# Kernel tuning notes

Measured on AMD Instinct MI355X. Metric: run time of the kernel, lower is better.

The kernel has to match this reference:

```python
import jax, jax.numpy as jnp
import numpy as np
import math

T = 2048; HID = 2048; H = 16; KV = 8; G = H // KV; D = 128
GH = 128; BS = 64; NB = T // BS
EPS = 1e-6; RATIO = 0.2; SCALE = 1.0 / math.sqrt(D)


def _rope_tables(length, dim, theta=1000000.0):
    inv = 1.0 / (theta ** (np.arange(0, dim, 2, dtype=np.float32) / dim))
    f = np.outer(np.arange(length, dtype=np.float32), inv)
    emb = np.concatenate([f, f], axis=-1)
    return jnp.asarray(np.cos(emb)), jnp.asarray(np.sin(emb))


def _rot_half(x):
    d = x.shape[-1] // 2
    return jnp.concatenate([-x[..., d:], x[..., :d]], axis=-1)


def _apply_rope(x, cos, sin):
    # x: [T, nH, D], cos/sin: [T, D] broadcast over head dim
    return x * cos[:, None, :] + _rot_half(x) * sin[:, None, :]


def _rmsnorm(x, w, eps=EPS):
    xf = x.astype(jnp.float32)
    v = jnp.mean(xf * xf, axis=-1, keepdims=True)
    return (w * (xf * jax.lax.rsqrt(v + eps))).astype(x.dtype)


def setup_inputs() -> dict:
    key = jax.random.key(0)
    ks = jax.random.split(key, 8)
    s = 0.02
    hidden_states = jax.random.normal(ks[0], (T, HID), jnp.float32)
    Wq = jax.random.normal(ks[1], (HID, H * D), jnp.float32) * s
    Wk = jax.random.normal(ks[2], (HID, KV * D), jnp.float32) * s
    Wv = jax.random.normal(ks[3], (HID, KV * D), jnp.float32) * s
    Wo = jax.random.normal(ks[4], (H * D, HID), jnp.float32) * s
    q_norm_w = jnp.ones((D,), jnp.float32)
    k_norm_w = jnp.ones((D,), jnp.float32)
    gate_wq = jax.random.normal(ks[5], (D, GH), jnp.float32) * s
    gate_wk = jax.random.normal(ks[6], (D, GH), jnp.float32) * s
    cos, sin = _rope_tables(T, D)
    cos_gq, sin_gq = _rope_tables(T, GH)
    cos_blk, sin_blk = _rope_tables(NB, GH)
    # causal block mask: query t may attend to key block j iff j <= t // BS
    block_attention_mask = (jnp.arange(T)[:, None] // BS) >= jnp.arange(NB)[None, :]
    return dict(hidden_states=hidden_states, Wq=Wq, Wk=Wk, Wv=Wv, Wo=Wo,
                q_norm_w=q_norm_w, k_norm_w=k_norm_w, gate_wq=gate_wq, gate_wk=gate_wk,
                cos=cos, sin=sin, cos_gq=cos_gq, sin_gq=sin_gq,
                cos_blk=cos_blk, sin_blk=sin_blk,
                block_attention_mask=block_attention_mask)


def reference(hidden_states, Wq, Wk, Wv, Wo, q_norm_w, k_norm_w, gate_wq, gate_wk,
              cos, sin, cos_gq, sin_gq, cos_blk, sin_blk, block_attention_mask):
    q = (hidden_states @ Wq).reshape(T, H, D)
    k = (hidden_states @ Wk).reshape(T, KV, D)
    v = (hidden_states @ Wv).reshape(T, KV, D)
    q = _rmsnorm(q, q_norm_w)
    k = _rmsnorm(k, k_norm_w)

    # ---- gate network on un-roped q/k: q-head avg-pool to KV heads, k avg-pool per block ----
    q_pool = q.reshape(T, KV, G, D).mean(axis=2)            # [T, KV, D]
    gq = _apply_rope(q_pool @ gate_wq, cos_gq, sin_gq)      # [T, KV, GH]
    k_blk = k.reshape(NB, BS, KV, D).mean(axis=1)           # [NB, KV, D]
    gk = _apply_rope(k_blk @ gate_wk, cos_blk, sin_blk)     # [NB, KV, GH]
    gate_scores = jnp.einsum('tkg,nkg->ktn', gq, gk) / math.sqrt(GH)  # [KV, T, NB]
    predict_mask = jnp.where(block_attention_mask[None], gate_scores, -1e9)

    # ---- main attention (RoPE + GQA causal softmax attention) ----
    qr = _apply_rope(q, cos, sin)
    kr = _apply_rope(k, cos, sin)
    kr_rep = jnp.repeat(kr, G, axis=1)                      # [T, H, D]
    v_rep = jnp.repeat(v, G, axis=1)
    logits = jnp.einsum('thd,shd->hts', qr, kr_rep) * SCALE  # [H, T, T]
    causal = jnp.tril(jnp.ones((T, T), bool))
    logits = jnp.where(causal[None], logits, -jnp.inf)
    probs = jax.nn.softmax(logits, axis=-1)
    attn_output = jnp.einsum('hts,shd->thd', probs, v_rep).reshape(T, H * D) @ Wo

    # ---- pooled ground-truth block mask: attention mass per key block ----
    pooled = probs.reshape(H, T, NB, BS).sum(axis=-1)        # [H, T, NB]
    gt = pooled.reshape(KV, G, T, NB).max(axis=1)            # max_pool3d over head groups -> [KV,T,NB]
    gt = jnp.where(block_attention_mask[None], gt, 0.0)
    gt = gt / (gt.sum(axis=-1, keepdims=True) + 1e-9)

    # ---- KLDiv gate loss on the tail slice (bsz = 1) ----
    start = int(T * RATIO)
    tgt = gt[:, start:, :]                                   # [KV, L, NB]
    logp = jax.nn.log_softmax(predict_mask[:, start:, :], axis=-1)
    safe_t = jnp.where(tgt > 0, tgt, 1.0)
    kl = jnp.where(tgt > 0, tgt * (jnp.log(safe_t) - logp), 0.0)
    gate_loss = kl.reshape(KV, -1).mean(axis=-1).sum()       # KLDivLoss(reduction='mean') per kv head, summed, /bsz(=1)
    return attn_output, gate_loss
```

## Files before the change

### kernel.cpp

```cpp
#include <hip/hip_runtime.h>

#define T_ 2048
#define HID_ 2048
#define H_ 16
#define KV_ 8
#define G_ 2
#define D_ 128
#define GH_ 128
#define BS_ 64
#define NB_ 32
#define START_ 409
#define TG0_ 384
#define SCALE_ 0.08838834764831845f
#define MFIX_ 8.0f

typedef __attribute__((ext_vector_type(8))) short short8_t;
typedef __attribute__((ext_vector_type(4))) float float4_t;
typedef __attribute__((ext_vector_type(8))) unsigned short ushort8_t;
typedef __attribute__((ext_vector_type(4))) unsigned short ushort4_t;

__device__ __forceinline__ float wave_sum(float v) {
#pragma unroll
  for (int o = 32; o > 0; o >>= 1) v += __shfl_xor(v, o, 64);
  return v;
}
__device__ __forceinline__ unsigned short f2bf(float x) {
  unsigned int u = __float_as_uint(x);
  unsigned int r = (u + 0x7fffu + ((u >> 16) & 1u)) >> 16;
  return (unsigned short)r;
}

__device__ __forceinline__ void gload16(const void* g, void* l) {
  __builtin_amdgcn_global_load_lds((const __attribute__((address_space(1))) unsigned int*)g,
                                   (__attribute__((address_space(3))) unsigned int*)l, 16, 0, 0);
}

__device__ __forceinline__ void castT_dev(const float* __restrict__ in,
                                          unsigned short* __restrict__ out, int K, int N,
                                          int ldin, int bx, int by,
                                          unsigned short (*tile)[72], int tid) {
  int k0 = by * 64, n0 = bx * 64;
  int tx = tid & 63, ty4 = tid >> 6;
#pragma unroll
  for (int i = 0; i < 16; ++i) {
    int ky = ty4 * 16 + i;
    tile[tx][ky] = f2bf(in[(size_t)(k0 + ky) * ldin + n0 + tx]);
  }
  __syncthreads();
#pragma unroll
  for (int i = 0; i < 16; ++i) {
    int ny = ty4 * 16 + i;
    out[(size_t)(n0 + ny) * K + k0 + tx] = tile[ny][tx];
  }
}

__global__ __launch_bounds__(256) void castT(const float* __restrict__ in,
                                             unsigned short* __restrict__ out,
                                             int K, int N, int ldin) {
  __shared__ unsigned short tile[64][72];
  castT_dev(in, out, K, N, ldin, blockIdx.x, blockIdx.y, tile, threadIdx.x);
}

__global__ __launch_bounds__(256) void prep_cast(const float* __restrict__ hs,
                                                 const float* __restrict__ Wq,
                                                 const float* __restrict__ Wk,
                                                 const float* __restrict__ Wv,
                                                 const float* __restrict__ Wo,
                                                 const float* __restrict__ gwq,
                                                 const float* __restrict__ gwk,
                                                 unsigned short* __restrict__ hsb,
                                                 unsigned short* __restrict__ WqkvT,
                                                 unsigned short* __restrict__ WoT,
                                                 unsigned short* __restrict__ gwqT,
                                                 unsigned short* __restrict__ gwkT) {
  __shared__ unsigned short tile[64][72];
  int id = blockIdx.x, tid = threadIdx.x;
  if (id < 4096) {
    int i = id * 256 + tid;
    float4 v = ((const float4*)hs)[i];
    ushort4_t o = {f2bf(v.x), f2bf(v.y), f2bf(v.z), f2bf(v.w)};
    *(ushort4_t*)(hsb + (size_t)i * 4) = o;
  } else if (id < 5120) {
    int t = id - 4096;
    castT_dev(Wq, WqkvT, 2048, 2048, 2048, t & 31, t >> 5, tile, tid);
  } else if (id < 5632) {
    int t = id - 5120;
    castT_dev(Wk, WqkvT + (size_t)2048 * 2048, 2048, 1024, 1024, t & 15, t >> 4, tile, tid);
  } else if (id < 6144) {
    int t = id - 5632;
    castT_dev(Wv, WqkvT + (size_t)3072 * 2048, 2048, 1024, 1024, t & 15, t >> 4, tile, tid);
  } else if (id < 7168) {
    int t = id - 6144;
    castT_dev(Wo, WoT, 2048, 2048, 2048, t & 31, t >> 5, tile, tid);
  } else if (id < 7172) {
    int t = id - 7168;
    castT_dev(gwq, gwqT, 128, 128, 128, t & 1, t >> 1, tile, tid);
  } else {
    int t = id - 7172;
    castT_dev(gwk, gwkT, 128, 128, 128, t & 1, t >> 1, tile, tid);
  }
}

__device__ __forceinline__ void gemm_body(const unsigned short* __restrict__ A,
                                          const unsigned short* __restrict__ Bt,
                                          float* __restrict__ C,
                                          int M, int N, int K, int ldc, int bx, int by,
                                          unsigned short* As, unsigned short* Bs) {
  int tid = threadIdx.x;
  int wid = tid >> 6, lane = tid & 63;
  int quad = lane >> 4, l16 = lane & 15;
  int wm = wid & 1, wn = wid >> 1;
  int m0 = by * 128, n0 = bx * 128;
  const unsigned short* gA[4];
  const unsigned short* gB[4];
#pragma unroll
  for (int it = 0; it < 4; ++it) {
    int line = wid * 32 + it * 8 + (lane >> 3);
    int chunk = (lane & 7) ^ (line & 7);
    gA[it] = A + (size_t)(m0 + line) * K + chunk * 8;
    gB[it] = Bt + (size_t)(n0 + line) * K + chunk * 8;
  }
  float4_t acc[4][4];
#pragma unroll
  for (int i = 0; i < 4; ++i)
#pragma unroll
    for (int j = 0; j < 4; ++j) acc[i][j] = (float4_t){0.f, 0.f, 0.f, 0.f};
  int nk = K >> 6;
#pragma unroll
  for (int it = 0; it < 4; ++it) {
    gload16(gA[it], As + (wid * 32 + it * 8) * 64);
    gload16(gB[it], Bs + (wid * 32 + it * 8) * 64);
  }
  for (int t = 0; t < nk; ++t) {
    __syncthreads();
    if (t + 1 < nk) {
      int bo = ((t + 1) & 1) * 8192;
#pragma unroll
      for (int it = 0; it < 4; ++it) {
        gload16(gA[it] + (t + 1) * 64, As + bo + (wid * 32 + it * 8) * 64);
        gload16(gB[it] + (t + 1) * 64, Bs + bo + (wid * 32 + it * 8) * 64);
      }
    }
    const unsigned short* Asc = As + (t & 1) * 8192;
    const unsigned short* Bsc = Bs + (t & 1) * 8192;
    short8_t a[2][4], b[2][4];
#pragma unroll
    for (int ks = 0; ks < 2; ++ks) {
      int sw = ((ks * 4 + quad) ^ (l16 & 7)) * 8;
#pragma unroll
      for (int i = 0; i < 4; ++i) {
        a[ks][i] = *(const short8_t*)&Asc[(wm * 64 + i * 16 + l16) * 64 + sw];
        b[ks][i] = *(const short8_t*)&Bsc[(wn * 64 + i * 16 + l16) * 64 + sw];
      }
    }
#pragma unroll
    for (int ks = 0; ks < 2; ++ks)
#pragma unroll
      for (int i = 0; i < 4; ++i)
#pragma unroll
        for (int j = 0; j < 4; ++j)
          acc[i][j] = __builtin_amdgcn_mfma_f32_16x16x32_bf16(a[ks][i], b[ks][j], acc[i][j], 0, 0, 0);
  }
#pragma unroll
  for (int i = 0; i < 4; ++i)
#pragma unroll
    for (int j = 0; j < 4; ++j)
#pragma unroll
      for (int reg = 0; reg < 4; ++reg)
        C[(size_t)(m0 + wm * 64 + i * 16 + quad * 4 + reg) * ldc + n0 + wn * 64 + j * 16 + l16] =
            acc[i][j][reg];
}

__global__ __launch_bounds__(256) void gemm_bf16_v3(const unsigned short* __restrict__ A,
                                                    const unsigned short* __restrict__ Bt,
                                                    float* __restrict__ C,
                                                    int M, int N, int K, int ldc) {
  __shared__ unsigned short As[2 * 128 * 64];
  __shared__ unsigned short Bs[2 * 128 * 64];
  gemm_body(A, Bt, C, M, N, K, ldc, blockIdx.x, blockIdx.y, As, Bs);
}

__global__ __launch_bounds__(256) void gemm_gates(const unsigned short* __restrict__ Aq,
                                                  const unsigned short* __restrict__ Bq,
                                                  float* __restrict__ Cq,
                                                  const unsigned short* __restrict__ Ak,
                                                  const unsigned short* __restrict__ Bk,
                                                  float* __restrict__ Ck) {
  __shared__ unsigned short As[2 * 128 * 64];
  __shared__ unsigned short Bs[2 * 128 * 64];
  int y = blockIdx.y;
  if (y < 104)
    gemm_body(Aq, Bq, Cq, 13312, 128, 128, 128, 0, y, As, Bs);
  else
    gemm_body(Ak, Bk, Ck, 256, 128, 128, 128, 0, y - 104, As, Bs);
}

__global__ __launch_bounds__(128) void norm_rope_fused(const float* __restrict__ qkvf,
                                                       const float* __restrict__ qw,
                                                       const float* __restrict__ kw,
                                                       const float* __restrict__ cosT,
                                                       const float* __restrict__ sinT,
                                                       unsigned short* __restrict__ qbf,
                                                       unsigned short* __restrict__ qpool_bf,
                                                       unsigned short* __restrict__ kbf,
                                                       float* __restrict__ knorm) {
  int t = blockIdx.x, d = threadIdx.x;
  if (blockIdx.y < 8) {
    int kv = blockIdx.y;
    size_t i0 = (size_t)t * 4096 + (kv * G_) * D_ + d;
    float x0 = qkvf[i0], x1 = qkvf[i0 + D_];
    __shared__ float sred[2][2];
    float s0 = wave_sum(x0 * x0), s1 = wave_sum(x1 * x1);
    if ((d & 63) == 0) { sred[0][d >> 6] = s0; sred[1][d >> 6] = s1; }
    __syncthreads();
    float wv = qw[d];
    float n0 = x0 * rsqrtf((sred[0][0] + sred[0][1]) * (1.f / D_) + 1e-6f) * wv;
    float n1 = x1 * rsqrtf((sred[1][0] + sred[1][1]) * (1.f / D_) + 1e-6f) * wv;
    if (t >= TG0_) qpool_bf[((size_t)(t - TG0_) * KV_ + kv) * D_ + d] = f2bf(0.5f * (n0 + n1));
    __shared__ float sh[2][D_];
    sh[0][d] = n0; sh[1][d] = n1;
    __syncthreads();
    float c = cosT[t * D_ + d], s = sinT[t * D_ + d];
    float r0 = (d < 64) ? -sh[0][d + 64] : sh[0][d - 64];
    float r1 = (d < 64) ? -sh[1][d + 64] : sh[1][d - 64];
    qbf[((size_t)(t * H_) + kv * G_) * D_ + d] = f2bf(n0 * c + r0 * s);
    qbf[((size_t)(t * H_) + kv * G_ + 1) * D_ + d] = f2bf(n1 * c + r1 * s);
  } else {
    int kv = blockIdx.y - 8;
    float x = qkvf[(size_t)t * 4096 + 2048 + kv * D_ + d];
    __shared__ float sredk[2];
    float s0 = wave_sum(x * x);
    if ((d & 63) == 0) sredk[d >> 6] = s0;
    __syncthreads();
    float nk = x * rsqrtf((sredk[0] + sredk[1]) * (1.f / D_) + 1e-6f) * kw[d];
    knorm[(size_t)(t * KV_ + kv) * D_ + d] = nk;
    __shared__ float shk[D_];
    shk[d] = nk;
    __syncthreads();
    float rot = (d < 64) ? -shk[d + 64] : shk[d - 64];
    kbf[(size_t)(t * KV_ + kv) * D_ + d] = f2bf(nk * cosT[t * D_ + d] + rot * sinT[t * D_ + d]);
  }
}

__global__ __launch_bounds__(128) void kblk_kernel(const float* __restrict__ knorm,
                                                   unsigned short* __restrict__ kblk_bf) {
  int n = blockIdx.x, kv = blockIdx.y, d = threadIdx.x;
  float s = 0.f;
  for (int i = 0; i < BS_; ++i) s += knorm[((size_t)(n * BS_ + i) * KV_ + kv) * D_ + d];
  kblk_bf[(size_t)(n * KV_ + kv) * D_ + d] = f2bf(s * (1.f / BS_));
}

__global__ __launch_bounds__(128) void rope_g_fused(float* __restrict__ gq, float* __restrict__ gk,
                                                    const float* __restrict__ cosG,
                                                    const float* __restrict__ sinG,
                                                    const float* __restrict__ cosB,
                                                    const float* __restrict__ sinB) {
  int r = blockIdx.x, kvh = blockIdx.y, d = threadIdx.x;
  float* x;
  size_t base;
  float c_, s_;
  if (r < NB_) {
    x = gk;
    base = (size_t)(r * KV_ + kvh) * GH_;
    c_ = cosB[r * GH_ + d]; s_ = sinB[r * GH_ + d];
  } else {
    int rr = r - NB_;
    x = gq;
    base = (size_t)(rr * KV_ + kvh) * GH_;
    c_ = cosG[(size_t)(TG0_ + rr) * GH_ + d]; s_ = sinG[(size_t)(TG0_ + rr) * GH_ + d];
  }
  __shared__ float sh[GH_];
  sh[d] = x[base + d];
  __syncthreads();
  float rot = (d < 64) ? -sh[d + 64] : sh[d - 64];
  x[base + d] = sh[d] * c_ + rot * s_;
}

__global__ __launch_bounds__(256, 2) void attn_mfma(const unsigned short* __restrict__ qbf,
                                                    const unsigned short* __restrict__ kbf,
                                                    const unsigned short* __restrict__ vt,
                                                    float* __restrict__ pooled,
                                                    float* __restrict__ o_acc,
                                                    float* __restrict__ l_acc) {
  int kv = blockIdx.x;
  int yy = blockIdx.y;
  int tile, c_lo, c_hi;
  if (yy < 32) { tile = yy;      c_lo = 0;                c_hi = (tile + 2) >> 1; }
  else         { tile = 63 - yy; c_lo = (tile + 2) >> 1;  c_hi = tile + 1; }
  int t0 = tile * 64;
  int tid = threadIdx.x;
  int wid = tid >> 6, lane = tid & 63;
  int quad = lane >> 4, l16 = lane & 15;
  __shared__ unsigned short Ks[2][64 * 128];
  __shared__ unsigned short Vs[2][128 * 64];
  __shared__ unsigned short Ps[8][16 * 64];

  const unsigned short* kbase[4];
  const unsigned short* vbase[4];
#pragma unroll
  for (int it = 0; it < 4; ++it) {
    int seg = wid * 4 + it;
    int krow = seg * 4 + (lane >> 4);
    int kchk = lane & 15;
    kbase[it] = kbf + ((size_t)krow * KV_ + kv) * D_ + ((kchk ^ (krow & 7)) << 3);
    int vrow = seg * 8 + (lane >> 3);
    int vchk = lane & 7;
    vbase[it] = vt + (size_t)(kv * 128 + vrow) * T_ + ((vchk ^ (vrow & 7)) << 3);
  }

  int tq = t0 + wid * 16 + l16;
  short8_t qf[2][4];
#pragma unroll
  for (int hh = 0; hh < 2; ++hh)
#pragma unroll
    for (int kb = 0; kb < 4; ++kb)
      qf[hh][kb] = *(const short8_t*)&qbf[((size_t)tq * H_ + kv * G_ + hh) * D_ + kb * 32 + quad * 8];

  const short one_bf = (short)0x3F80;
  short8_t ones = {one_bf, one_bf, one_bf, one_bf, one_bf, one_bf, one_bf, one_bf};

  int tbase = t0 + wid * 16 + quad * 4;
  float l_[2][4] = {};
  float pacc[2][2][4] = {};
  float4_t o[2][8];
#pragma unroll
  for (int hh = 0; hh < 2; ++hh)
#pragma unroll
    for (int j = 0; j < 8; ++j) o[hh][j] = (float4_t){0.f, 0.f, 0.f, 0.f};

#pragma unroll
  for (int it = 0; it < 4; ++it) {
    gload16(kbase[it] + (size_t)c_lo * 65536, &Ks[c_lo & 1][(wid * 4 + it) * 512]);
    gload16(vbase[it] + c_lo * 64, &Vs[c_lo & 1][(wid * 4 + it) * 512]);
  }
  for (int c = c_lo; c < c_hi; ++c) {
    __syncthreads();
    if (c + 1 < c_hi) {
      int b = (c + 1) & 1;
#pragma unroll
      for (int it = 0; it < 4; ++it) {
        gload16(kbase[it] + (size_t)(c + 1) * 65536, &Ks[b][(wid * 4 + it) * 512]);
        gload16(vbase[it] + (c + 1) * 64, &Vs[b][(wid * 4 + it) * 512]);
      }
    }
    const unsigned short* Ksc = Ks[c & 1];
    const unsigned short* Vsc = Vs[c & 1];
    int half = c >> 4, cl = c & 15;

    float4_t s[2][4];
#pragma unroll
    for (int j = 0; j < 4; ++j) {
      float4_t a0 = (float4_t){0.f, 0.f, 0.f, 0.f};
      float4_t a1 = (float4_t){0.f, 0.f, 0.f, 0.f};
#pragma unroll
      for (int kb = 0; kb < 4; ++kb) {
        short8_t kf = *(const short8_t*)&Ksc[(j * 16 + l16) * 128 + (((kb * 4 + quad) ^ (l16 & 7)) << 3)];
        a0 = __builtin_amdgcn_mfma_f32_16x16x32_bf16(qf[0][kb], kf, a0, 0, 0, 0);
        a1 = __builtin_amdgcn_mfma_f32_16x16x32_bf16(qf[1][kb], kf, a1, 0, 0, 0);
      }
      s[0][j] = a0;
      s[1][j] = a1;
    }
#pragma unroll
    for (int hh = 0; hh < 2; ++hh) {
      if (c == tile) {
#pragma unroll
        for (int reg = 0; reg < 4; ++reg) {
          int trow = tbase + reg;
#pragma unroll
          for (int j = 0; j < 4; ++j) {
            float p = __expf(s[hh][j][reg] * SCALE_ - MFIX_);
            s[hh][j][reg] = (c * 64 + j * 16 + l16 <= trow) ? p : 0.f;
          }
        }
      } else {
#pragma unroll
        for (int j = 0; j < 4; ++j)
#pragma unroll
          for (int reg = 0; reg < 4; ++reg)
            s[hh][j][reg] = __expf(s[hh][j][reg] * SCALE_ - MFIX_);
      }
#pragma unroll
      for (int j = 0; j < 4; ++j)
#pragma unroll
        for (int reg = 0; reg < 4; ++reg) {
          int r = quad * 4 + reg;
          Ps[wid * 2 + hh][r * 64 + ((j * 16 + l16) ^ ((r & 7) << 3))] = f2bf(s[hh][j][reg]);
        }
    }
    float4_t pool[2] = {(float4_t){0.f, 0.f, 0.f, 0.f}, (float4_t){0.f, 0.f, 0.f, 0.f}};
#pragma unroll
    for (int ks = 0; ks < 2; ++ks) {
      int psw = l16 * 64 + (((ks * 4 + quad) ^ (l16 & 7)) << 3);
      short8_t pf0 = *(const short8_t*)&Ps[wid * 2 + 0][psw];
      short8_t pf1 = *(const short8_t*)&Ps[wid * 2 + 1][psw];
      pool[0] = __builtin_amdgcn_mfma_f32_16x16x32_bf16(pf0, ones, pool[0], 0, 0, 0);
      pool[1] = __builtin_amdgcn_mfma_f32_16x16x32_bf16(pf1, ones, pool[1], 0, 0, 0);
#pragma unroll
      for (int jt = 0; jt < 8; ++jt) {
        short8_t vf = *(const short8_t*)&Vsc[(jt * 16 + l16) * 64 + (((ks * 4 + quad) ^ (l16 & 7)) << 3)];
        o[0][jt] = __builtin_amdgcn_mfma_f32_16x16x32_bf16(pf0, vf, o[0][jt], 0, 0, 0);
        o[1][jt] = __builtin_amdgcn_mfma_f32_16x16x32_bf16(pf1, vf, o[1][jt], 0, 0, 0);
      }
    }
#pragma unroll
    for (int hh = 0; hh < 2; ++hh)
#pragma unroll
      for (int reg = 0; reg < 4; ++reg) {
        l_[hh][reg] += pool[hh][reg];
        if (l16 == cl) pacc[hh][half][reg] = pool[hh][reg];
      }
  }
#pragma unroll
  for (int hh = 0; hh < 2; ++hh) {
    int h = kv * G_ + hh;
#pragma unroll
    for (int reg = 0; reg < 4; ++reg) {
      int trow = tbase + reg;
      if (l16 >= c_lo && l16 < c_hi)
        pooled[((size_t)h * T_ + trow) * NB_ + l16] = pacc[hh][0][reg];
      if (16 + l16 >= c_lo && 16 + l16 < c_hi)
        pooled[((size_t)h * T_ + trow) * NB_ + 16 + l16] = pacc[hh][1][reg];
    }
#pragma unroll
    for (int jt = 0; jt < 8; ++jt)
#pragma unroll
      for (int reg = 0; reg < 4; ++reg)
        atomicAdd(&o_acc[(((size_t)h * T_) + tbase + reg) * D_ + jt * 16 + l16], o[hh][jt][reg]);
    if (l16 == 0) {
#pragma unroll
      for (int reg = 0; reg < 4; ++reg)
        atomicAdd(&l_acc[(size_t)h * T_ + tbase + reg], l_[hh][reg]);
    }
  }
}

__device__ __forceinline__ void gate_loss_body(const float* __restrict__ gq,
                                               const float* __restrict__ gk,
                                               const float* __restrict__ pooled,
                                               const float* __restrict__ l_acc,
                                               float* __restrict__ klsum,
                                               int kv, int yblk, float4* gks4) {
  int tid = threadIdx.x;
#pragma unroll
  for (int p = 0; p < 4; ++p) {
    int f = p * 256 + tid;
    int n = f >> 5, d4 = f & 31;
    gks4[n * 32 + (d4 ^ (n & 7))] =
        *(const float4*)(gk + ((size_t)n * KV_ + kv) * GH_ + d4 * 4);
  }
  __syncthreads();
  int sub = tid >> 5;
  int n = tid & 31;
  int tloc = yblk * 8 + sub;
  bool act = tloc < (T_ - START_);
  int t = START_ + (act ? tloc : 0);
  const float4* a = (const float4*)(gq + ((size_t)(t - TG0_) * KV_ + kv) * GH_);
  float dot = 0.f;
#pragma unroll
  for (int d4 = 0; d4 < 32; ++d4) {
    float4 av = a[d4];
    float4 bv = gks4[n * 32 + (d4 ^ (n & 7))];
    dot += av.x * bv.x + av.y * bv.y + av.z * bv.z + av.w * bv.w;
  }
  bool valid = (t / BS_) >= n;
  float score = valid ? dot * SCALE_ : -1e9f;
  float M = score;
#pragma unroll
  for (int o = 16; o > 0; o >>= 1) M = fmaxf(M, __shfl_xor(M, o, 64));
  float e = __expf(score - M);
  float Z = e;
#pragma unroll
  for (int o = 16; o > 0; o >>= 1) Z += __shfl_xor(Z, o, 64);
  float logZ = M + logf(Z);
  float g = 0.f;
  if (valid) {
    float rl0 = 1.f / l_acc[(size_t)(kv * G_) * T_ + t];
    float rl1 = 1.f / l_acc[(size_t)(kv * G_ + 1) * T_ + t];
    float p0 = pooled[((size_t)(kv * G_) * T_ + t) * NB_ + n] * rl0;
    float p1 = pooled[((size_t)(kv * G_ + 1) * T_ + t) * NB_ + n] * rl1;
    g = fmaxf(p0, p1);
  }
  float gs = g;
#pragma unroll
  for (int o = 16; o > 0; o >>= 1) gs += __shfl_xor(gs, o, 64);
  float tgt = g / (gs + 1e-9f);
  float kl = (tgt > 0.f) ? tgt * (logf(tgt) - (score - logZ)) : 0.f;
  float ks = kl;
#pragma unroll
  for (int o = 16; o > 0; o >>= 1) ks += __shfl_xor(ks, o, 64);
  if (n == 0 && act) klsum[kv * (T_ - START_) + tloc] = ks;
}

__global__ __launch_bounds__(256) void combine_gate(const float* __restrict__ o_acc,
                                                    const float* __restrict__ l_acc,
                                                    unsigned short* __restrict__ attnb,
                                                    const float* __restrict__ gq,
                                                    const float* __restrict__ gk,
                                                    const float* __restrict__ pooled,
                                                    float* __restrict__ klsum) {
  __shared__ float4 gks4[1024];
  int id = blockIdx.x;
  if (id < 1640) {
    gate_loss_body(gq, gk, pooled, l_acc, klsum, id & 7, id >> 3, gks4);
  } else {
    int gid = (id - 1640) * 256 + threadIdx.x;
    int row = gid >> 5, q4 = gid & 31;
    int h = row >> 11, t = row & 2047;
    float inv = 1.f / l_acc[row];
    float4 a = ((const float4*)o_acc)[gid];
    ushort4_t ov = {f2bf(a.x * inv), f2bf(a.y * inv), f2bf(a.z * inv), f2bf(a.w * inv)};
    *(ushort4_t*)(attnb + (size_t)t * (H_ * D_) + h * D_ + q4 * 4) = ov;
  }
}

__global__ __launch_bounds__(256) void finalize_loss(const float* __restrict__ klsum,
                                                     float* __restrict__ out) {
  const int n = KV_ * (T_ - START_);
  float s = 0.f;
  for (int i = threadIdx.x; i < n; i += 256) s += klsum[i];
  s = wave_sum(s);
  __shared__ float sh[4];
  if ((threadIdx.x & 63) == 0) sh[threadIdx.x >> 6] = s;
  __syncthreads();
  if (threadIdx.x == 0)
    out[0] = (sh[0] + sh[1] + sh[2] + sh[3]) * (1.f / ((float)(T_ - START_) * NB_));
}

extern "C" void kernel_launch(void* const* d_in, const int* in_sizes, int n_in,
                              void* d_out, int out_size, void* d_ws, size_t ws_size,
                              hipStream_t stream) {
  const float* hs   = (const float*)d_in[0];
  const float* Wq   = (const float*)d_in[1];
  const float* Wk   = (const float*)d_in[2];
  const float* Wv   = (const float*)d_in[3];
  const float* Wo   = (const float*)d_in[4];
  const float* qw   = (const float*)d_in[5];
  const float* kw   = (const float*)d_in[6];
  const float* gwq  = (const float*)d_in[7];
  const float* gwk  = (const float*)d_in[8];
  const float* cosT = (const float*)d_in[9];
  const float* sinT = (const float*)d_in[10];
  const float* cosG = (const float*)d_in[11];
  const float* sinG = (const float*)d_in[12];
  const float* cosB = (const float*)d_in[13];
  const float* sinB = (const float*)d_in[14];
  float* out = (float*)d_out;
  float* ws = (float*)d_ws;
  const size_t MEG = 1048576;

  float*          qkvf     = ws;
  unsigned short* attnb    = (unsigned short*)ws;
  float*          pooled   = ws + 2 * MEG;
  float*          klsum    = ws + 3 * MEG;
  float*          l_acc    = ws + 3 * MEG + 65536;
  float*          o_acc    = ws + 4 * MEG;
  unsigned short* WqkvT    = (unsigned short*)(ws + 8 * MEG);
  unsigned short* qbf      = WqkvT;
  unsigned short* kbf      = WqkvT + 4 * MEG;
  unsigned short* vt       = WqkvT + 6 * MEG;
  unsigned short* hsb      = (unsigned short*)(ws + 12 * MEG);
  float*          knorm    = ws + 12 * MEG;
  unsigned short* WoT      = (unsigned short*)(ws + 14 * MEG);
  unsigned short* qpool_bf = (unsigned short*)(ws + 16 * MEG);
  float*          gq       = ws + 17 * MEG;
  unsigned short* kblk_bf  = (unsigned short*)(ws + 18 * MEG + 786432);
  float*          gk       = ws + 18 * MEG + 819200;
  unsigned short* gwqT     = (unsigned short*)(ws + 18 * MEG + 851968);
  unsigned short* gwkT     = (unsigned short*)(ws + 18 * MEG + 860160);

  prep_cast<<<7176, 256, 0, stream>>>(hs, Wq, Wk, Wv, Wo, gwq, gwk, hsb, WqkvT, WoT, gwqT, gwkT);
  gemm_bf16_v3<<<dim3(32, 16), 256, 0, stream>>>(hsb, WqkvT, qkvf, 2048, 4096, 2048, 4096);
  norm_rope_fused<<<dim3(T_, 16), 128, 0, stream>>>(qkvf, qw, kw, cosT, sinT, qbf, qpool_bf,
                                                    kbf, knorm);
  castT<<<dim3(16, 32), 256, 0, stream>>>(qkvf + 3072, vt, T_, 1024, 4096);
  hipMemsetAsync(o_acc, 0, (size_t)4 * MEG * sizeof(float), stream);
  hipMemsetAsync(l_acc, 0, (size_t)H_ * T_ * sizeof(float), stream);
  kblk_kernel<<<dim3(NB_, KV_), 128, 0, stream>>>(knorm, kblk_bf);
  gemm_gates<<<dim3(1, 106), 256, 0, stream>>>(qpool_bf, gwqT, gq, kblk_bf, gwkT, gk);
  rope_g_fused<<<dim3(NB_ + (T_ - TG0_), KV_), 128, 0, stream>>>(gq, gk, cosG, sinG, cosB, sinB);
  attn_mfma<<<dim3(KV_, 64), 256, 0, stream>>>(qbf, kbf, vt, pooled, o_acc, l_acc);
  combine_gate<<<1640 + 4096, 256, 0, stream>>>(o_acc, l_acc, attnb, gq, gk, pooled, klsum);
  gemm_bf16_v3<<<dim3(16, 16), 256, 0, stream>>>(attnb, WoT, out, 2048, 2048, 2048, 2048);
  finalize_loss<<<1, 256, 0, stream>>>(klsum, out + (size_t)T_ * HID_);
}
```

Before: 321.4 us.

## Split attention query tiles into balanced key chunks and fuse castT with kblk

The attention grid now splits each causal query tile into chunks of at most eight key blocks, replacing the paired half-split. This gives 80 work items per kv head instead of 64, with a shorter maximum per-block workload. The V transpose-cast and the key block-mean kernels are merged into one launch to save a kernel launch. More chunks mean more atomic accumulation into the partial output and normalizer buffers.

```diff
diff --git a/kernel.cpp b/kernel.cpp
--- a/kernel.cpp
+++ b/kernel.cpp
@@ -52,13 +52,6 @@
     int ny = ty4 * 16 + i;
     out[(size_t)(n0 + ny) * K + k0 + tx] = tile[ny][tx];
   }
-}
-
-__global__ __launch_bounds__(256) void castT(const float* __restrict__ in,
-                                             unsigned short* __restrict__ out,
-                                             int K, int N, int ldin) {
-  __shared__ unsigned short tile[64][72];
-  castT_dev(in, out, K, N, ldin, blockIdx.x, blockIdx.y, tile, threadIdx.x);
 }
 
 __global__ __launch_bounds__(256) void prep_cast(const float* __restrict__ hs,
@@ -242,12 +235,21 @@
   }
 }
 
-__global__ __launch_bounds__(128) void kblk_kernel(const float* __restrict__ knorm,
-                                                   unsigned short* __restrict__ kblk_bf) {
-  int n = blockIdx.x, kv = blockIdx.y, d = threadIdx.x;
-  float s = 0.f;
-  for (int i = 0; i < BS_; ++i) s += knorm[((size_t)(n * BS_ + i) * KV_ + kv) * D_ + d];
-  kblk_bf[(size_t)(n * KV_ + kv) * D_ + d] = f2bf(s * (1.f / BS_));
+__global__ __launch_bounds__(256) void castT_kblk(const float* __restrict__ qkvf,
+                                                  unsigned short* __restrict__ vt,
+                                                  const float* __restrict__ knorm,
+                                                  unsigned short* __restrict__ kblk_bf) {
+  __shared__ unsigned short tile[64][72];
+  int id = blockIdx.x, tid = threadIdx.x;
+  if (id < 512) {
+    castT_dev(qkvf + 3072, vt, T_, 1024, 4096, id & 15, id >> 4, tile, tid);
+  } else {
+    int task = (id - 512) * 2 + (tid >> 7);
+    int n = task >> 3, kv = task & 7, d = tid & 127;
+    float s = 0.f;
+    for (int i = 0; i < BS_; ++i) s += knorm[((size_t)(n * BS_ + i) * KV_ + kv) * D_ + d];
+    kblk_bf[(size_t)(n * KV_ + kv) * D_ + d] = f2bf(s * (1.f / BS_));
+  }
 }
 
 __global__ __launch_bounds__(128) void rope_g_fused(float* __restrict__ gq, float* __restrict__ gk,
@@ -283,10 +285,23 @@
                                                     float* __restrict__ o_acc,
                                                     float* __restrict__ l_acc) {
   int kv = blockIdx.x;
-  int yy = blockIdx.y;
-  int tile, c_lo, c_hi;
-  if (yy < 32) { tile = yy;      c_lo = 0;                c_hi = (tile + 2) >> 1; }
-  else         { tile = 63 - yy; c_lo = (tile + 2) >> 1;  c_hi = tile + 1; }
+  int y = blockIdx.y;
+  int tile = 0, c_lo = 0, c_hi = 0;
+  {
+    int acc = 0;
+    for (int t = 0; t < 32; ++t) {
+      int n = t + 1, p = (n + 7) >> 3;
+      if (y < acc + p) {
+        int pi = y - acc;
+        int base = n / p, rem = n % p;
+        c_lo = pi * base + (pi < rem ? pi : rem);
+        c_hi = c_lo + base + (pi < rem ? 1 : 0);
+        tile = t;
+        break;
+      }
+      acc += p;
+    }
+  }
   int t0 = tile * 64;
   int tid = threadIdx.x;
   int wid = tid >> 6, lane = tid & 63;
@@ -573,13 +588,12 @@
   gemm_bf16_v3<<<dim3(32, 16), 256, 0, stream>>>(hsb, WqkvT, qkvf, 2048, 4096, 2048, 4096);
   norm_rope_fused<<<dim3(T_, 16), 128, 0, stream>>>(qkvf, qw, kw, cosT, sinT, qbf, qpool_bf,
                                                     kbf, knorm);
-  castT<<<dim3(16, 32), 256, 0, stream>>>(qkvf + 3072, vt, T_, 1024, 4096);
+  castT_kblk<<<640, 256, 0, stream>>>(qkvf, vt, knorm, kblk_bf);
   hipMemsetAsync(o_acc, 0, (size_t)4 * MEG * sizeof(float), stream);
   hipMemsetAsync(l_acc, 0, (size_t)H_ * T_ * sizeof(float), stream);
-  kblk_kernel<<<dim3(NB_, KV_), 128, 0, stream>>>(knorm, kblk_bf);
   gemm_gates<<<dim3(1, 106), 256, 0, stream>>>(qpool_bf, gwqT, gq, kblk_bf, gwkT, gk);
   rope_g_fused<<<dim3(NB_ + (T_ - TG0_), KV_), 128, 0, stream>>>(gq, gk, cosG, sinG, cosB, sinB);
-  attn_mfma<<<dim3(KV_, 64), 256, 0, stream>>>(qbf, kbf, vt, pooled, o_acc, l_acc);
+  attn_mfma<<<dim3(KV_, 80), 256, 0, stream>>>(qbf, kbf, vt, pooled, o_acc, l_acc);
   combine_gate<<<1640 + 4096, 256, 0, stream>>>(o_acc, l_acc, attnb, gq, gk, pooled, klsum);
   gemm_bf16_v3<<<dim3(16, 16), 256, 0, stream>>>(attnb, WoT, out, 2048, 2048, 2048, 2048);
   finalize_loss<<<1, 256, 0, stream>>>(klsum, out + (size_t)T_ * HID_);
```

New measurement: 335.8 us. 1.04x slower.
